# Performance work log

Measured on AMD Instinct MI355X. Metric: run time of the kernel, lower is better.

Reference implementation:

```python
import jax, jax.numpy as jnp
import numpy as np

N = 4096      # nodes
E = 131072    # edges
C_IN = 128
HID = 128     # d_model of transformer (= embed_dim used in reshape_to_trans)
OUT = 32      # GNN output channels -> transformer seq_len
HEADS = 8
DH = HID // HEADS
FF = 2048     # torch TransformerEncoderLayer default dim_feedforward
EPS = 1e-5


def layer_norm(x, g, b):
    mu = jnp.mean(x, axis=-1, keepdims=True)
    var = jnp.mean(jnp.square(x - mu), axis=-1, keepdims=True)
    return (x - mu) * jax.lax.rsqrt(var + EPS) * g + b


def setup_inputs() -> dict:
    key = jax.random.key(0)
    ks = jax.random.split(key, 24)
    def rn(k, shape, scale=0.05):
        return jax.random.normal(k, shape, dtype=jnp.float32) * scale
    inp = {
        "x": jax.random.normal(ks[0], (N, C_IN), dtype=jnp.float32),
        "edge_index": jax.random.randint(ks[1], (2, E), 0, N, dtype=jnp.int64),
        # GCN layers
        "Wg1": rn(ks[2], (C_IN, HID)), "bg1": jnp.zeros((HID,), jnp.float32),
        "Wg2": rn(ks[3], (HID, HID)),  "bg2": jnp.zeros((HID,), jnp.float32),
        "Wg3": rn(ks[4], (HID, OUT)),  "bg3": jnp.zeros((OUT,), jnp.float32),
        # MHA
        "Wq": rn(ks[5], (HID, HID)), "bq": jnp.zeros((HID,), jnp.float32),
        "Wk": rn(ks[6], (HID, HID)), "bk": jnp.zeros((HID,), jnp.float32),
        "Wv": rn(ks[7], (HID, HID)), "bv": jnp.zeros((HID,), jnp.float32),
        "Wo": rn(ks[8], (HID, HID)), "bo": jnp.zeros((HID,), jnp.float32),
        "ln1_g": jnp.ones((HID,), jnp.float32), "ln1_b": jnp.zeros((HID,), jnp.float32),
        # FFN
        "W1": rn(ks[9], (HID, FF)),  "b1": jnp.zeros((FF,), jnp.float32),
        "W2": rn(ks[10], (FF, HID)), "b2": jnp.zeros((HID,), jnp.float32),
        "ln2_g": jnp.ones((HID,), jnp.float32), "ln2_b": jnp.zeros((HID,), jnp.float32),
    }
    return inp


def reference(x, edge_index, Wg1, bg1, Wg2, bg2, Wg3, bg3,
              Wq, bq, Wk, bk, Wv, bv, Wo, bo, ln1_g, ln1_b,
              W1, b1, W2, b2, ln2_g, ln2_b):
    # ---- GCN normalization (add self-loops, symmetric D^-1/2 (A+I) D^-1/2) ----
    loop = jnp.arange(N, dtype=edge_index.dtype)
    src = jnp.concatenate([edge_index[0], loop])
    dst = jnp.concatenate([edge_index[1], loop])
    deg = jax.ops.segment_sum(jnp.ones((E + N,), jnp.float32), dst, num_segments=N)
    dinv = jnp.where(deg > 0, jax.lax.rsqrt(deg), 0.0)
    norm = (dinv[src] * dinv[dst])[:, None]  # [E+N, 1]

    def gcn(h, W, b):
        m = h @ W                               # [N, d_out]
        agg = jax.ops.segment_sum(m[src] * norm, dst, num_segments=N)
        return agg + b

    h = jax.nn.relu(gcn(x, Wg1, bg1))
    h = jax.nn.relu(gcn(h, Wg2, bg2))
    h = jax.nn.relu(gcn(h, Wg3, bg3))           # [N, OUT]

    # ---- reshape_to_trans: [N, OUT] -> [N, OUT, HID] (repeat along embed dim) ----
    t = jnp.broadcast_to(h[:, :, None], (N, OUT, HID))

    # ---- TransformerEncoderLayer (post-norm, relu FFN, no dropout at eval) ----
    q = (t @ Wq + bq).reshape(N, OUT, HEADS, DH)
    k = (t @ Wk + bk).reshape(N, OUT, HEADS, DH)
    v = (t @ Wv + bv).reshape(N, OUT, HEADS, DH)
    scores = jnp.einsum("bqhd,bkhd->bhqk", q, k) / jnp.sqrt(jnp.float32(DH))
    attn = jax.nn.softmax(scores, axis=-1)
    ctx = jnp.einsum("bhqk,bkhd->bqhd", attn, v).reshape(N, OUT, HID)
    a = ctx @ Wo + bo
    x1 = layer_norm(t + a, ln1_g, ln1_b)
    f = jax.nn.relu(x1 @ W1 + b1) @ W2 + b2
    out = layer_norm(x1 + f, ln2_g, ln2_b)      # [N, OUT, HID]
    return out
```

## Files before the change

kernel.cpp:

```cpp
#include <hip/hip_runtime.h>

#define NN 4096
#define EE 131072
#define FFD 2048

typedef float f32x4 __attribute__((ext_vector_type(4)));
typedef __bf16 bf16x8 __attribute__((ext_vector_type(8)));
typedef unsigned int u32;
typedef u32 u32x4 __attribute__((ext_vector_type(4)));
typedef unsigned short u16;
typedef u16 u16x8 __attribute__((ext_vector_type(8)));

__device__ __forceinline__ u16 f2bf(float f) {
    unsigned u = __builtin_bit_cast(unsigned, f);
    return (u16)((u + 0x7FFFu + ((u >> 16) & 1u)) >> 16);
}
__device__ __forceinline__ float bf2f(u16 h) {
    unsigned u = ((unsigned)h) << 16;
    return __builtin_bit_cast(float, u);
}
__device__ __forceinline__ u32 pk2bf(float lo, float hi) {
    return (u32)f2bf(lo) | ((u32)f2bf(hi) << 16);
}

#define GLD16(g, l) __builtin_amdgcn_global_load_lds(                            \
    (const __attribute__((address_space(1))) void*)(g),                          \
    (__attribute__((address_space(3))) void*)(l), 16, 0, 0)

__global__ void k_detect(const int* __restrict__ ei, int* __restrict__ flag) {
    int v = ei[2 * threadIdx.x + 1];
    unsigned long long any = __ballot(v != 0);
    if (threadIdx.x == 0) *flag = (any == 0ULL) ? 1 : 0;
}
__device__ __forceinline__ int ldedge(const int* ei, int idx, int is64) {
    return is64 ? ei[2 * idx] : ei[idx];
}

__global__ void k_degi(const int* __restrict__ ei, const int* __restrict__ flag,
                       int* __restrict__ cnt) {
    int e = blockIdx.x * 256 + threadIdx.x;
    if (e >= EE) return;
    atomicAdd(&cnt[ldedge(ei, EE + e, *flag)], 1);
}
__global__ void k_dinv(const int* __restrict__ cnt, float* __restrict__ dinv) {
    int n = blockIdx.x * 256 + threadIdx.x;
    if (n < NN) dinv[n] = rsqrtf((float)cnt[n] + 1.0f);
}
__global__ __launch_bounds__(1024) void k_scan(const int* __restrict__ cnt,
        int* __restrict__ rp, int* __restrict__ cur) {
    __shared__ int tsum[1024];
    int t = threadIdx.x;
    int c0 = cnt[t * 4], c1 = cnt[t * 4 + 1], c2 = cnt[t * 4 + 2], c3 = cnt[t * 4 + 3];
    int s = c0 + c1 + c2 + c3;
    tsum[t] = s;
    __syncthreads();
    for (int off = 1; off < 1024; off <<= 1) {
        int v = (t >= off) ? tsum[t - off] : 0;
        __syncthreads();
        tsum[t] += v;
        __syncthreads();
    }
    int excl = tsum[t] - s;
    int p0 = excl, p1 = excl + c0, p2 = p1 + c1, p3 = p2 + c2;
    rp[t * 4] = p0; rp[t * 4 + 1] = p1; rp[t * 4 + 2] = p2; rp[t * 4 + 3] = p3;
    cur[t * 4] = p0; cur[t * 4 + 1] = p1; cur[t * 4 + 2] = p2; cur[t * 4 + 3] = p3;
    if (t == 1023) rp[4096] = excl + s;
}
__global__ void k_bucket(const int* __restrict__ ei, const int* __restrict__ flag,
                         int* __restrict__ cur, int* __restrict__ es) {
    int e = blockIdx.x * 256 + threadIdx.x;
    if (e >= EE) return;
    int is64 = *flag;
    int s = ldedge(ei, e, is64), d = ldedge(ei, EE + e, is64);
    int pos = atomicAdd(&cur[d], 1);
    es[pos] = s;
}

__global__ __launch_bounds__(256) void k_gcn_mm128(const float* __restrict__ h,
        const float* __restrict__ W, const float* __restrict__ dinv, float* __restrict__ ms) {
    __shared__ float hr[2][128];
    int t = threadIdx.x, n0 = blockIdx.x * 2, r = t >> 7, e = t & 127;
    hr[r][e] = h[(size_t)(n0 + r) * 128 + e];
    __syncthreads();
    float a = 0.f;
    #pragma unroll 8
    for (int c = 0; c < 128; ++c) a += hr[r][c] * W[c * 128 + e];
    ms[(size_t)(n0 + r) * 128 + e] = a * dinv[n0 + r];
}
__global__ __launch_bounds__(256) void k_gcn_mm32(const float* __restrict__ h,
        const float* __restrict__ W, const float* __restrict__ dinv, float* __restrict__ ms) {
    __shared__ float hr[8][128];
    int t = threadIdx.x, n0 = blockIdx.x * 8;
    for (int k2 = 0; k2 < 4; ++k2) {
        int idx = k2 * 256 + t;
        hr[idx >> 7][idx & 127] = h[(size_t)n0 * 128 + idx];
    }
    __syncthreads();
    int r = t >> 5, e = t & 31;
    float a = 0.f;
    #pragma unroll 8
    for (int c = 0; c < 128; ++c) a += hr[r][c] * W[c * 32 + e];
    ms[(size_t)(n0 + r) * 32 + e] = a * dinv[n0 + r];
}

__global__ __launch_bounds__(256) void k_gath128(const int* __restrict__ es,
        const int* __restrict__ rp, const float* __restrict__ ms,
        const float* __restrict__ dinv, const float* __restrict__ b,
        float* __restrict__ hout) {
    int node = blockIdx.x * 4 + (threadIdx.x >> 6), lane = threadIdx.x & 63;
    int st = rp[node], en = rp[node + 1];
    const float2* m2 = (const float2*)ms;
    float ax0 = 0.f, ay0 = 0.f, ax1 = 0.f, ay1 = 0.f;
    int e = st;
    for (; e + 2 <= en; e += 2) {
        int s0 = es[e], s1 = es[e + 1];
        float2 v0 = m2[(size_t)s0 * 64 + lane];
        float2 v1 = m2[(size_t)s1 * 64 + lane];
        ax0 += v0.x; ay0 += v0.y; ax1 += v1.x; ay1 += v1.y;
    }
    if (e < en) {
        float2 v = m2[(size_t)es[e] * 64 + lane];
        ax0 += v.x; ay0 += v.y;
    }
    float dv = dinv[node];
    float2 self = m2[(size_t)node * 64 + lane];
    int c = lane * 2;
    hout[(size_t)node * 128 + c]     = fmaxf(dv * (ax0 + ax1 + self.x) + b[c], 0.f);
    hout[(size_t)node * 128 + c + 1] = fmaxf(dv * (ay0 + ay1 + self.y) + b[c + 1], 0.f);
}
__global__ __launch_bounds__(256) void k_gath32(const int* __restrict__ es,
        const int* __restrict__ rp, const float* __restrict__ ms,
        const float* __restrict__ dinv, const float* __restrict__ b,
        float* __restrict__ hout) {
    int node = blockIdx.x * 8 + (threadIdx.x >> 5), sl = threadIdx.x & 31;
    int st = rp[node], en = rp[node + 1];
    float a0 = 0.f, a1 = 0.f;
    int e = st;
    for (; e + 2 <= en; e += 2) {
        a0 += ms[(size_t)es[e] * 32 + sl];
        a1 += ms[(size_t)es[e + 1] * 32 + sl];
    }
    if (e < en) a0 += ms[(size_t)es[e] * 32 + sl];
    float dv = dinv[node];
    hout[(size_t)node * 32 + sl] =
        fmaxf(dv * (a0 + a1 + ms[(size_t)node * 32 + sl]) + b[sl], 0.f);
}

__global__ __launch_bounds__(128) void k_prep(const float* __restrict__ Wq, const float* __restrict__ bq,
        const float* __restrict__ Wk, const float* __restrict__ bk,
        const float* __restrict__ Wv, const float* __restrict__ bv,
        const float* __restrict__ Wo, const float* __restrict__ bo, float* __restrict__ tc) {
    __shared__ float s_q[128], s_k[128], s_v[128];
    int t = threadIdx.x;
    float aq = 0, ak = 0, av = 0;
    for (int c = 0; c < 128; ++c) {
        aq += Wq[c * 128 + t]; ak += Wk[c * 128 + t]; av += Wv[c * 128 + t];
    }
    s_q[t] = aq; s_k[t] = ak; s_v[t] = av;
    tc[t] = aq; tc[128 + t] = ak; tc[256 + t] = av;
    __syncthreads();
    float pb = 0;
    for (int d = 0; d < 128; ++d) pb += bv[d] * Wo[d * 128 + t];
    tc[1440 + t] = pb + bo[t];
    for (int hh = 0; hh < 8; ++hh) {
        float p = 0;
        #pragma unroll
        for (int d = hh * 16; d < hh * 16 + 16; ++d) p += s_v[d] * Wo[d * 128 + t];
        tc[416 + hh * 128 + t] = p;
    }
    if (t < 8) {
        float A = 0, B = 0, C = 0, D = 0;
        #pragma unroll
        for (int d = t * 16; d < t * 16 + 16; ++d) {
            A += s_q[d] * s_k[d]; B += s_q[d] * bk[d];
            C += bq[d] * s_k[d];  D += bq[d] * bk[d];
        }
        tc[384 + t] = A; tc[392 + t] = B; tc[400 + t] = C; tc[408 + t] = D;
    }
}

__global__ void k_w1t(const float* __restrict__ W1, u16* __restrict__ w1t) {
    int t = blockIdx.x * 256 + threadIdx.x;
    int f = t >> 7, c = t & 127;
    w1t[t] = f2bf(W1[c * 2048 + f]);
}
__global__ void k_w2t(const float* __restrict__ W2, u16* __restrict__ w2t) {
    int t = blockIdx.x * 256 + threadIdx.x;
    int o = t >> 11, f = t & 2047;
    w2t[t] = f2bf(W2[f * 128 + o]);
}

__global__ __launch_bounds__(256) void k_attn(const float* __restrict__ h3, const float* __restrict__ tc,
        const float* __restrict__ g1, const float* __restrict__ b1n, float* __restrict__ x1) {
    __shared__ float sh[32];
    __shared__ float ws_[8][32];
    int n = blockIdx.x, t = threadIdx.x;
    if (t < 32) sh[t] = h3[(size_t)n * 32 + t];
    __syncthreads();
    {
        int hh = t >> 5, i = t & 31;
        float A = tc[384 + hh], C = tc[400 + hh];
        float coef = (sh[i] * A + C) * 0.25f;
        float m = -1e30f;
        #pragma unroll
        for (int j = 0; j < 32; ++j) m = fmaxf(m, coef * sh[j]);
        float s = 0.f, wsum = 0.f;
        #pragma unroll
        for (int j = 0; j < 32; ++j) {
            float e = __expf(coef * sh[j] - m);
            s += e; wsum += e * sh[j];
        }
        ws_[hh][i] = wsum / s;
    }
    __syncthreads();
    int wave = t >> 6, lane = t & 63;
    float pb0 = tc[1440 + lane], pb1 = tc[1440 + lane + 64];
    float po0[8], po1[8];
    #pragma unroll
    for (int hh = 0; hh < 8; ++hh) {
        po0[hh] = tc[416 + hh * 128 + lane];
        po1[hh] = tc[416 + hh * 128 + lane + 64];
    }
    float ga = g1[lane], gb = g1[lane + 64], ba = b1n[lane], bb = b1n[lane + 64];
    for (int i = wave; i < 32; i += 4) {
        float y0 = sh[i] + pb0, y1 = sh[i] + pb1;
        #pragma unroll
        for (int hh = 0; hh < 8; ++hh) {
            float w = ws_[hh][i];
            y0 += w * po0[hh]; y1 += w * po1[hh];
        }
        float s1 = y0 + y1, s2 = y0 * y0 + y1 * y1;
        #pragma unroll
        for (int off = 1; off < 64; off <<= 1) {
            s1 += __shfl_xor(s1, off); s2 += __shfl_xor(s2, off);
        }
        float mu = s1 * (1.f / 128.f);
        float var = s2 * (1.f / 128.f) - mu * mu;
        float rs = rsqrtf(var + 1e-5f);
        size_t base = ((size_t)n * 32 + i) * 128;
        x1[base + lane]      = (y0 - mu) * rs * ga + ba;
        x1[base + lane + 64] = (y1 - mu) * rs * gb + bb;
    }
}


#define STAGE(buf, Fb) {                                                         \
    char* db_ = (char*)(buf);                                                    \
    _Pragma("unroll") for (int c1_ = 0; c1_ < 4; ++c1_) {                        \
        int f_ = c1_ * 16 + (t >> 4);                                            \
        int bo_ = ((t & 15) * 16) ^ ((f_ & 7) << 4);                             \
        GLD16(w1t + (size_t)((Fb) + f_) * 128 + (bo_ >> 1),                      \
              db_ + c1_ * 4096 + wave * 1024);                                   \
    }                                                                            \
    _Pragma("unroll") for (int c2_ = 0; c2_ < 4; ++c2_) {                        \
        int o_ = c2_ * 32 + (t >> 3);                                            \
        int bo_ = ((t & 7) * 16) ^ ((o_ & 7) << 4);                              \
        GLD16(w2t + (size_t)o_ * 2048 + (Fb) + (bo_ >> 1),                       \
              db_ + 16384 + c2_ * 4096 + wave * 1024);                           \
    } }

#define FCOMP(buf, Fb) {                                                         \
    const char* wb_ = (const char*)(buf);                                        \
    _Pragma("unroll") for (int cf_ = 0; cf_ < 4; ++cf_) {                        \
        bf16x8 w1f_[4];                                                          \
        _Pragma("unroll") for (int ks_ = 0; ks_ < 4; ++ks_)                      \
            w1f_[ks_] = *(const bf16x8*)(wb_ + (cf_ * 16 + li) * 256 +           \
                ((ks_ * 64 + g * 16) ^ ((li & 7) << 4)));                        \
        f32x4 a0_ = (f32x4){0.f, 0.f, 0.f, 0.f};                                 \
        f32x4 a1_ = (f32x4){0.f, 0.f, 0.f, 0.f};                                 \
        _Pragma("unroll") for (int ks_ = 0; ks_ < 4; ++ks_) {                    \
            a0_ = __builtin_amdgcn_mfma_f32_16x16x32_bf16(af[0][ks_], w1f_[ks_], a0_, 0, 0, 0); \
            a1_ = __builtin_amdgcn_mfma_f32_16x16x32_bf16(af[1][ks_], w1f_[ks_], a1_, 0, 0, 0); \
        }                                                                        \
        float bias_ = b1[(Fb) + cf_ * 16 + li];                                  \
        _Pragma("unroll") for (int r_ = 0; r_ < 4; ++r_) {                       \
            int row0_ = g * 4 + r_;                                              \
            int row1_ = 16 + g * 4 + r_;                                         \
            *(u16*)(hwb + ((row0_ * 128 + (cf_ * 16 + li) * 2) ^ ((row0_ & 7) << 4))) \
                = f2bf(fmaxf(a0_[r_] + bias_, 0.f));                             \
            *(u16*)(hwb + ((row1_ * 128 + (cf_ * 16 + li) * 2) ^ ((row1_ & 7) << 4))) \
                = f2bf(fmaxf(a1_[r_] + bias_, 0.f));                             \
        }                                                                        \
    }                                                                            \
    _Pragma("unroll") for (int k2_ = 0; k2_ < 2; ++k2_) {                        \
        bf16x8 a2_[2];                                                           \
        _Pragma("unroll") for (int rf_ = 0; rf_ < 2; ++rf_) {                    \
            int row_ = rf_ * 16 + li;                                            \
            a2_[rf_] = *(const bf16x8*)(hwb +                                    \
                ((row_ * 128 + (k2_ * 32 + g * 8) * 2) ^ ((row_ & 7) << 4)));    \
        }                                                                        \
        _Pragma("unroll") for (int c2_ = 0; c2_ < 8; ++c2_) {                    \
            bf16x8 w2f_ = *(const bf16x8*)(wb_ + 16384 + (c2_ * 16 + li) * 128 + \
                ((k2_ * 64 + g * 16) ^ ((li & 7) << 4)));                        \
            acc2[0][c2_] = __builtin_amdgcn_mfma_f32_16x16x32_bf16(a2_[0], w2f_, acc2[0][c2_], 0, 0, 0); \
            acc2[1][c2_] = __builtin_amdgcn_mfma_f32_16x16x32_bf16(a2_[1], w2f_, acc2[1][c2_], 0, 0, 0); \
        }                                                                        \
    } }

__global__ __launch_bounds__(256, 3) void k_ffn(const float* x1f, const u16* __restrict__ w1t,
        const u16* __restrict__ w2t, const float* __restrict__ b1, const float* __restrict__ b2,
        const float* __restrict__ g2, const float* __restrict__ bt2, float* out) {
    __shared__ u16 wA[16384];
    __shared__ u16 hid[4][32 * 64];
    int t = threadIdx.x, wave = t >> 6, lane = t & 63;
    int g = lane >> 4, li = lane & 15;
    size_t rowbase = (size_t)blockIdx.x * 128;
    char* hwb = (char*)&hid[wave][0];

    STAGE(wA, 0);

    bf16x8 af[2][4];
    #pragma unroll
    for (int rf = 0; rf < 2; ++rf)
    #pragma unroll
    for (int ks = 0; ks < 4; ++ks) {
        const float* p = x1f + (rowbase + wave * 32 + rf * 16 + li) * 128 + ks * 32 + g * 8;
        float4 v0 = *(const float4*)(p);
        float4 v1 = *(const float4*)(p + 4);
        u32x4 q = { pk2bf(v0.x, v0.y), pk2bf(v0.z, v0.w),
                    pk2bf(v1.x, v1.y), pk2bf(v1.z, v1.w) };
        af[rf][ks] = __builtin_bit_cast(bf16x8, q);
    }

    f32x4 acc2[2][8];
    #pragma unroll
    for (int a = 0; a < 2; ++a)
    #pragma unroll
    for (int b = 0; b < 8; ++b) acc2[a][b] = (f32x4){0.f, 0.f, 0.f, 0.f};

    __syncthreads();

    for (int F = 0; F < FFD; F += 64) {
        FCOMP(wA, F);
        __syncthreads();
        if (F + 64 < FFD) {
            STAGE(wA, F + 64);
            __syncthreads();
        }
    }

    #pragma unroll
    for (int rf = 0; rf < 2; ++rf)
    #pragma unroll
    for (int r = 0; r < 4; ++r) {
        int lrow = wave * 32 + rf * 16 + g * 4 + r;
        size_t grow = rowbase + lrow;
        float vals[8], s1 = 0.f, s2 = 0.f;
        #pragma unroll
        for (int cf2 = 0; cf2 < 8; ++cf2) {
            int col = cf2 * 16 + li;
            float xv = bf2f(f2bf(x1f[grow * 128 + col]));
            float y = xv + acc2[rf][cf2][r] + b2[col];
            vals[cf2] = y; s1 += y; s2 += y * y;
        }
        #pragma unroll
        for (int m = 1; m < 16; m <<= 1) {
            s1 += __shfl_xor(s1, m); s2 += __shfl_xor(s2, m);
        }
        float mu = s1 * (1.f / 128.f);
        float var = s2 * (1.f / 128.f) - mu * mu;
        float rs = rsqrtf(var + 1e-5f);
        #pragma unroll
        for (int cf2 = 0; cf2 < 8; ++cf2) {
            int col = cf2 * 16 + li;
            out[grow * 128 + col] = (vals[cf2] - mu) * rs * g2[col] + bt2[col];
        }
    }
}

extern "C" void kernel_launch(void* const* d_in, const int* in_sizes, int n_in,
                              void* d_out, int out_size, void* d_ws, size_t ws_size,
                              hipStream_t stream) {
    const float* x   = (const float*)d_in[0];
    const int*   ei  = (const int*)d_in[1];
    const float *Wg1 = (const float*)d_in[2],  *bg1 = (const float*)d_in[3];
    const float *Wg2 = (const float*)d_in[4],  *bg2 = (const float*)d_in[5];
    const float *Wg3 = (const float*)d_in[6],  *bg3 = (const float*)d_in[7];
    const float *Wq  = (const float*)d_in[8],  *bq  = (const float*)d_in[9];
    const float *Wk  = (const float*)d_in[10], *bk  = (const float*)d_in[11];
    const float *Wv  = (const float*)d_in[12], *bv  = (const float*)d_in[13];
    const float *Wo  = (const float*)d_in[14], *bo  = (const float*)d_in[15];
    const float *g1  = (const float*)d_in[16], *b1n = (const float*)d_in[17];
    const float *W1  = (const float*)d_in[18], *b1  = (const float*)d_in[19];
    const float *W2  = (const float*)d_in[20], *b2  = (const float*)d_in[21];
    const float *g2  = (const float*)d_in[22], *bt2 = (const float*)d_in[23];

    char* ws = (char*)d_ws;
    int*   flag = (int*)(ws + 0);
    int*   cnt  = (int*)(ws + 4096);
    int*   rp   = (int*)(ws + 20480);
    int*   cur  = (int*)(ws + 40960);
    float* dinv = (float*)(ws + 57344);
    float* ms   = (float*)(ws + 73728);
    int*   es   = (int*)(ws + 2170880);
    float* hA   = (float*)(ws + 2695168);
    float* hB   = (float*)(ws + 4792320);
    float* tc   = (float*)(ws + 6889472);
    u16*   w1t  = (u16*)(ws + 6897664);
    u16*   w2t  = (u16*)(ws + 7421952);
    float* x1   = (float*)d_out;
    float* out  = (float*)d_out;

    k_detect<<<1, 64, 0, stream>>>(ei, flag);
    hipMemsetAsync(cnt, 0, 16384, stream);
    k_degi<<<512, 256, 0, stream>>>(ei, flag, cnt);
    k_dinv<<<16, 256, 0, stream>>>(cnt, dinv);
    k_scan<<<1, 1024, 0, stream>>>(cnt, rp, cur);
    k_bucket<<<512, 256, 0, stream>>>(ei, flag, cur, es);

    k_gcn_mm128<<<2048, 256, 0, stream>>>(x, Wg1, dinv, ms);
    k_gath128<<<1024, 256, 0, stream>>>(es, rp, ms, dinv, bg1, hA);
    k_gcn_mm128<<<2048, 256, 0, stream>>>(hA, Wg2, dinv, ms);
    k_gath128<<<1024, 256, 0, stream>>>(es, rp, ms, dinv, bg2, hB);
    k_gcn_mm32<<<512, 256, 0, stream>>>(hB, Wg3, dinv, ms);
    k_gath32<<<512, 256, 0, stream>>>(es, rp, ms, dinv, bg3, hA);

    k_prep<<<1, 128, 0, stream>>>(Wq, bq, Wk, bk, Wv, bv, Wo, bo, tc);
    k_w1t<<<1024, 256, 0, stream>>>(W1, w1t);
    k_w2t<<<1024, 256, 0, stream>>>(W2, w2t);

    k_attn<<<4096, 256, 0, stream>>>(hA, tc, g1, b1n, x1);

    k_ffn<<<1024, 256, 0, stream>>>(x1, w1t, w2t, b1, b2, g2, bt2, out);
}
```

Measured before the change: 338.2 us.

## Double-buffer FFN weight staging, store x1 as bf16, merge small prep kernels

Splits each 64-wide FFN chunk into two 32-wide halves held in separate LDS buffers, so global-to-LDS loads of the next half overlap the MFMA work on the current half. The LDS footprint drops, allowing four blocks per CU instead of three. The attention kernel now writes x1 as bf16 to workspace, which halves that intermediate's write and read traffic and removes the in-FFN conversion. The dinv computation is folded into the scan kernel and the two weight-transpose kernels are merged into one launch to cut launch overhead. Numerics are unchanged, because x1 was already rounded to bf16 before the FFN used it.

```diff
diff --git a/kernel.cpp b/kernel.cpp
--- a/kernel.cpp
+++ b/kernel.cpp
@@ -19,9 +19,6 @@
     unsigned u = ((unsigned)h) << 16;
     return __builtin_bit_cast(float, u);
 }
-__device__ __forceinline__ u32 pk2bf(float lo, float hi) {
-    return (u32)f2bf(lo) | ((u32)f2bf(hi) << 16);
-}
 
 #define GLD16(g, l) __builtin_amdgcn_global_load_lds(                            \
     (const __attribute__((address_space(1))) void*)(g),                          \
@@ -42,17 +39,17 @@
     if (e >= EE) return;
     atomicAdd(&cnt[ldedge(ei, EE + e, *flag)], 1);
 }
-__global__ void k_dinv(const int* __restrict__ cnt, float* __restrict__ dinv) {
-    int n = blockIdx.x * 256 + threadIdx.x;
-    if (n < NN) dinv[n] = rsqrtf((float)cnt[n] + 1.0f);
-}
 __global__ __launch_bounds__(1024) void k_scan(const int* __restrict__ cnt,
-        int* __restrict__ rp, int* __restrict__ cur) {
+        int* __restrict__ rp, int* __restrict__ cur, float* __restrict__ dinv) {
     __shared__ int tsum[1024];
     int t = threadIdx.x;
     int c0 = cnt[t * 4], c1 = cnt[t * 4 + 1], c2 = cnt[t * 4 + 2], c3 = cnt[t * 4 + 3];
     int s = c0 + c1 + c2 + c3;
     tsum[t] = s;
+    dinv[t * 4]     = rsqrtf((float)c0 + 1.0f);
+    dinv[t * 4 + 1] = rsqrtf((float)c1 + 1.0f);
+    dinv[t * 4 + 2] = rsqrtf((float)c2 + 1.0f);
+    dinv[t * 4 + 3] = rsqrtf((float)c3 + 1.0f);
     __syncthreads();
     for (int off = 1; off < 1024; off <<= 1) {
         int v = (t >= off) ? tsum[t - off] : 0;
@@ -179,19 +176,16 @@
     }
 }
 
-__global__ void k_w1t(const float* __restrict__ W1, u16* __restrict__ w1t) {
-    int t = blockIdx.x * 256 + threadIdx.x;
-    int f = t >> 7, c = t & 127;
-    w1t[t] = f2bf(W1[c * 2048 + f]);
-}
-__global__ void k_w2t(const float* __restrict__ W2, u16* __restrict__ w2t) {
-    int t = blockIdx.x * 256 + threadIdx.x;
-    int o = t >> 11, f = t & 2047;
-    w2t[t] = f2bf(W2[f * 128 + o]);
+__global__ void k_wt(const float* __restrict__ W1, const float* __restrict__ W2,
+                     u16* __restrict__ w1t, u16* __restrict__ w2t) {
+    int b = blockIdx.x;
+    int t = (b & 1023) * 256 + threadIdx.x;
+    if (b < 1024) { int f = t >> 7, c = t & 127; w1t[t] = f2bf(W1[c * 2048 + f]); }
+    else          { int o = t >> 11, f = t & 2047; w2t[t] = f2bf(W2[f * 128 + o]); }
 }
 
 __global__ __launch_bounds__(256) void k_attn(const float* __restrict__ h3, const float* __restrict__ tc,
-        const float* __restrict__ g1, const float* __restrict__ b1n, float* __restrict__ x1) {
+        const float* __restrict__ g1, const float* __restrict__ b1n, u16* __restrict__ x1b) {
     __shared__ float sh[32];
     __shared__ float ws_[8][32];
     int n = blockIdx.x, t = threadIdx.x;
@@ -238,30 +232,30 @@
         float var = s2 * (1.f / 128.f) - mu * mu;
         float rs = rsqrtf(var + 1e-5f);
         size_t base = ((size_t)n * 32 + i) * 128;
-        x1[base + lane]      = (y0 - mu) * rs * ga + ba;
-        x1[base + lane + 64] = (y1 - mu) * rs * gb + bb;
-    }
-}
-
-
-#define STAGE(buf, Fb) {                                                         \
+        x1b[base + lane]      = f2bf((y0 - mu) * rs * ga + ba);
+        x1b[base + lane + 64] = f2bf((y1 - mu) * rs * gb + bb);
+    }
+}
+
+
+#define STAGE32(buf, Fb) {                                                       \
     char* db_ = (char*)(buf);                                                    \
-    _Pragma("unroll") for (int c1_ = 0; c1_ < 4; ++c1_) {                        \
+    _Pragma("unroll") for (int c1_ = 0; c1_ < 2; ++c1_) {                        \
         int f_ = c1_ * 16 + (t >> 4);                                            \
         int bo_ = ((t & 15) * 16) ^ ((f_ & 7) << 4);                             \
         GLD16(w1t + (size_t)((Fb) + f_) * 128 + (bo_ >> 1),                      \
               db_ + c1_ * 4096 + wave * 1024);                                   \
     }                                                                            \
-    _Pragma("unroll") for (int c2_ = 0; c2_ < 4; ++c2_) {                        \
-        int o_ = c2_ * 32 + (t >> 3);                                            \
-        int bo_ = ((t & 7) * 16) ^ ((o_ & 7) << 4);                              \
+    _Pragma("unroll") for (int c2_ = 0; c2_ < 2; ++c2_) {                        \
+        int o_ = c2_ * 64 + (t >> 2);                                            \
+        int bo_ = ((t & 3) * 16) ^ ((o_ & 3) << 4);                              \
         GLD16(w2t + (size_t)o_ * 2048 + (Fb) + (bo_ >> 1),                       \
-              db_ + 16384 + c2_ * 4096 + wave * 1024);                           \
+              db_ + 8192 + c2_ * 4096 + wave * 1024);                            \
     } }
 
-#define FCOMP(buf, Fb) {                                                         \
+#define FCOMP32(buf, Fb) {                                                       \
     const char* wb_ = (const char*)(buf);                                        \
-    _Pragma("unroll") for (int cf_ = 0; cf_ < 4; ++cf_) {                        \
+    _Pragma("unroll") for (int cf_ = 0; cf_ < 2; ++cf_) {                        \
         bf16x8 w1f_[4];                                                          \
         _Pragma("unroll") for (int ks_ = 0; ks_ < 4; ++ks_)                      \
             w1f_[ks_] = *(const bf16x8*)(wb_ + (cf_ * 16 + li) * 256 +           \
@@ -276,51 +270,48 @@
         _Pragma("unroll") for (int r_ = 0; r_ < 4; ++r_) {                       \
             int row0_ = g * 4 + r_;                                              \
             int row1_ = 16 + g * 4 + r_;                                         \
-            *(u16*)(hwb + ((row0_ * 128 + (cf_ * 16 + li) * 2) ^ ((row0_ & 7) << 4))) \
+            *(u16*)(hwb + row0_ * 64 + (((cf_ * 16 + li) * 2) ^ ((row0_ & 6) << 3))) \
                 = f2bf(fmaxf(a0_[r_] + bias_, 0.f));                             \
-            *(u16*)(hwb + ((row1_ * 128 + (cf_ * 16 + li) * 2) ^ ((row1_ & 7) << 4))) \
+            *(u16*)(hwb + row1_ * 64 + (((cf_ * 16 + li) * 2) ^ ((row1_ & 6) << 3))) \
                 = f2bf(fmaxf(a1_[r_] + bias_, 0.f));                             \
         }                                                                        \
     }                                                                            \
-    _Pragma("unroll") for (int k2_ = 0; k2_ < 2; ++k2_) {                        \
+    {                                                                            \
         bf16x8 a2_[2];                                                           \
         _Pragma("unroll") for (int rf_ = 0; rf_ < 2; ++rf_) {                    \
             int row_ = rf_ * 16 + li;                                            \
-            a2_[rf_] = *(const bf16x8*)(hwb +                                    \
-                ((row_ * 128 + (k2_ * 32 + g * 8) * 2) ^ ((row_ & 7) << 4)));    \
+            a2_[rf_] = *(const bf16x8*)(hwb + row_ * 64 +                        \
+                ((g * 16) ^ ((li & 6) << 3)));                                   \
         }                                                                        \
         _Pragma("unroll") for (int c2_ = 0; c2_ < 8; ++c2_) {                    \
-            bf16x8 w2f_ = *(const bf16x8*)(wb_ + 16384 + (c2_ * 16 + li) * 128 + \
-                ((k2_ * 64 + g * 16) ^ ((li & 7) << 4)));                        \
+            bf16x8 w2f_ = *(const bf16x8*)(wb_ + 8192 + (c2_ * 16 + li) * 64 +   \
+                ((g * 16) ^ ((li & 3) << 4)));                                   \
             acc2[0][c2_] = __builtin_amdgcn_mfma_f32_16x16x32_bf16(a2_[0], w2f_, acc2[0][c2_], 0, 0, 0); \
             acc2[1][c2_] = __builtin_amdgcn_mfma_f32_16x16x32_bf16(a2_[1], w2f_, acc2[1][c2_], 0, 0, 0); \
         }                                                                        \
     } }
 
-__global__ __launch_bounds__(256, 3) void k_ffn(const float* x1f, const u16* __restrict__ w1t,
-        const u16* __restrict__ w2t, const float* __restrict__ b1, const float* __restrict__ b2,
-        const float* __restrict__ g2, const float* __restrict__ bt2, float* out) {
-    __shared__ u16 wA[16384];
-    __shared__ u16 hid[4][32 * 64];
+__global__ __launch_bounds__(256, 4) void k_ffn(const u16* __restrict__ x1b,
+        const u16* __restrict__ w1t, const u16* __restrict__ w2t,
+        const float* __restrict__ b1, const float* __restrict__ b2,
+        const float* __restrict__ g2, const float* __restrict__ bt2, float* __restrict__ out) {
+    __shared__ u16 wA[8192];
+    __shared__ u16 wB[8192];
+    __shared__ u16 hid[4][1024];
     int t = threadIdx.x, wave = t >> 6, lane = t & 63;
     int g = lane >> 4, li = lane & 15;
     size_t rowbase = (size_t)blockIdx.x * 128;
     char* hwb = (char*)&hid[wave][0];
 
-    STAGE(wA, 0);
+    STAGE32(wA, 0);
 
     bf16x8 af[2][4];
     #pragma unroll
     for (int rf = 0; rf < 2; ++rf)
     #pragma unroll
-    for (int ks = 0; ks < 4; ++ks) {
-        const float* p = x1f + (rowbase + wave * 32 + rf * 16 + li) * 128 + ks * 32 + g * 8;
-        float4 v0 = *(const float4*)(p);
-        float4 v1 = *(const float4*)(p + 4);
-        u32x4 q = { pk2bf(v0.x, v0.y), pk2bf(v0.z, v0.w),
-                    pk2bf(v1.x, v1.y), pk2bf(v1.z, v1.w) };
-        af[rf][ks] = __builtin_bit_cast(bf16x8, q);
-    }
+    for (int ks = 0; ks < 4; ++ks)
+        af[rf][ks] = *(const bf16x8*)(x1b +
+            (rowbase + wave * 32 + rf * 16 + li) * 128 + ks * 32 + g * 8);
 
     f32x4 acc2[2][8];
     #pragma unroll
@@ -331,12 +322,12 @@
     __syncthreads();
 
     for (int F = 0; F < FFD; F += 64) {
-        FCOMP(wA, F);
+        STAGE32(wB, F + 32);
+        FCOMP32(wA, F);
         __syncthreads();
-        if (F + 64 < FFD) {
-            STAGE(wA, F + 64);
-            __syncthreads();
-        }
+        if (F + 64 < FFD) STAGE32(wA, F + 64);
+        FCOMP32(wB, F + 32);
+        __syncthreads();
     }
 
     #pragma unroll
@@ -349,7 +340,7 @@
         #pragma unroll
         for (int cf2 = 0; cf2 < 8; ++cf2) {
             int col = cf2 * 16 + li;
-            float xv = bf2f(f2bf(x1f[grow * 128 + col]));
+            float xv = bf2f(x1b[grow * 128 + col]);
             float y = xv + acc2[rf][cf2][r] + b2[col];
             vals[cf2] = y; s1 += y; s2 += y * y;
         }
@@ -398,14 +389,13 @@
     float* tc   = (float*)(ws + 6889472);
     u16*   w1t  = (u16*)(ws + 6897664);
     u16*   w2t  = (u16*)(ws + 7421952);
-    float* x1   = (float*)d_out;
+    u16*   x1b  = (u16*)(ws + 8388608);
     float* out  = (float*)d_out;
 
     k_detect<<<1, 64, 0, stream>>>(ei, flag);
     hipMemsetAsync(cnt, 0, 16384, stream);
     k_degi<<<512, 256, 0, stream>>>(ei, flag, cnt);
-    k_dinv<<<16, 256, 0, stream>>>(cnt, dinv);
-    k_scan<<<1, 1024, 0, stream>>>(cnt, rp, cur);
+    k_scan<<<1, 1024, 0, stream>>>(cnt, rp, cur, dinv);
     k_bucket<<<512, 256, 0, stream>>>(ei, flag, cur, es);
 
     k_gcn_mm128<<<2048, 256, 0, stream>>>(x, Wg1, dinv, ms);
@@ -416,10 +406,9 @@
     k_gath32<<<512, 256, 0, stream>>>(es, rp, ms, dinv, bg3, hA);
 
     k_prep<<<1, 128, 0, stream>>>(Wq, bq, Wk, bk, Wv, bv, Wo, bo, tc);
-    k_w1t<<<1024, 256, 0, stream>>>(W1, w1t);
-    k_w2t<<<1024, 256, 0, stream>>>(W2, w2t);
-
-    k_attn<<<4096, 256, 0, stream>>>(hA, tc, g1, b1n, x1);
-
-    k_ffn<<<1024, 256, 0, stream>>>(x1, w1t, w2t, b1, b2, g2, bt2, out);
-}
+    k_wt<<<2048, 256, 0, stream>>>(W1, W2, w1t, w2t);
+
+    k_attn<<<4096, 256, 0, stream>>>(hA, tc, g1, b1n, x1b);
+
+    k_ffn<<<1024, 256, 0, stream>>>(x1b, w1t, w2t, b1, b2, g2, bt2, out);
+}
```

Result: slower. 594.9 us (+75.9%).
